# Performance work log

Measured on AMD Instinct MI355X. Metric: run time of the kernel, lower is better.

Reference implementation:

```python
import jax, jax.numpy as jnp
import numpy as np

B, H, S, DK, DV = 2, 16, 2048, 64, 64


def setup_inputs() -> dict:
    key = jax.random.key(0)
    kq, kk, kv = jax.random.split(key, 3)
    queries = jax.random.normal(kq, (B, H, S, DK), dtype=jnp.float32)
    keys = jax.random.normal(kk, (B, H, S, DK), dtype=jnp.float32)
    values = jax.random.normal(kv, (B, H, S, DV), dtype=jnp.float32)
    # causal boolean mask, broadcastable over batch and heads
    mask = jnp.tril(jnp.ones((S, S), dtype=bool))[None, None, :, :]
    return {"queries": queries, "keys": keys, "values": values, "d_k": DK, "mask": mask}


def reference(queries, keys, values, d_k, mask):
    scale = 1.0 / jnp.sqrt(jnp.float32(d_k))
    # scores: [B, H, S, S]
    scores = jnp.einsum("bhqd,bhkd->bhqk", queries, keys) * scale
    mask_f = mask.astype(jnp.float32)
    scores = scores + (-1e9) * (1.0 - mask_f)
    weights = jax.nn.softmax(scores, axis=-1)
    # second mask step from the original: min(|mask|, |weights|)
    weights = jnp.minimum(jnp.abs(mask_f), jnp.abs(weights))
    return jnp.einsum("bhqk,bhkd->bhqd", weights, values)
```

## Files before the change

kernel.cpp:

```cpp
#include <hip/hip_runtime.h>
#include <hip/hip_bf16.h>

#define B_ 2
#define H_ 16
#define S_ 2048
#define D_ 64

typedef __attribute__((ext_vector_type(8))) short bf16x8;
typedef __attribute__((ext_vector_type(8))) unsigned short u16x8;
typedef __attribute__((ext_vector_type(4))) unsigned int u32x4;
typedef __attribute__((ext_vector_type(4))) float f32x4;
typedef unsigned short ushort_t;

#define SCALE 0.18033688011112042f

__device__ __forceinline__ unsigned short f2bf(float x) {
  unsigned int u = __builtin_bit_cast(unsigned int, x);
  unsigned int r = (u + 0x7FFFu + ((u >> 16) & 1u)) >> 16;
  return (unsigned short)r;
}

__device__ __forceinline__ unsigned int cvt_pk_bf16(float lo, float hi) {
  unsigned int r;
  asm("v_cvt_pk_bf16_f32 %0, %1, %2" : "=v"(r) : "v"(lo), "v"(hi));
  return r;
}

__device__ __forceinline__ float fast_exp2(float x) {
  float r;
  asm("v_exp_f32 %0, %1" : "=v"(r) : "v"(x));
  return r;
}

__device__ __forceinline__ float fmax3(float a, float b, float c) {
  return fmaxf(fmaxf(a, b), c);
}

__device__ __forceinline__ int sigma_row(int rl) {
  return (rl & 0x23) | ((rl & 0x0C) << 1) | ((rl & 0x10) >> 2);
}

#define GLL16(gp, lp)                                                          \
  __builtin_amdgcn_global_load_lds(                                            \
      (const __attribute__((address_space(1))) unsigned int*)(gp),             \
      (__attribute__((address_space(3))) unsigned int*)(lp), 16, 0, 0)

__global__ void prepack(const float* __restrict__ Kf, const float* __restrict__ Vf,
                        ushort_t* __restrict__ Kg, ushort_t* __restrict__ Vtg) {
  const int blk = blockIdx.x;
  const int tid = threadIdx.x;
  const int bh = blk >> 5, t = blk & 31;
  const float* srcK = Kf + ((size_t)bh * S_ + (size_t)t * 64) * D_;
  const float* srcV = Vf + ((size_t)bh * S_ + (size_t)t * 64) * D_;
  ushort_t* dK = Kg + (size_t)blk * 4096;
  ushort_t* dV = Vtg + (size_t)blk * 4096;
  for (int is = 0; is < 2; ++is) {
    const int e = is * 2048 + tid * 8;
    {
      const int rl = e >> 6, pos = (e >> 3) & 7, ch = pos ^ (rl & 7);
      const float* sp = srcK + sigma_row(rl) * 64 + ch * 8;
      float4 a = *(const float4*)sp;
      float4 b = *(const float4*)(sp + 4);
      u16x8 w;
      w[0] = f2bf(a.x); w[1] = f2bf(a.y); w[2] = f2bf(a.z); w[3] = f2bf(a.w);
      w[4] = f2bf(b.x); w[5] = f2bf(b.y); w[6] = f2bf(b.z); w[7] = f2bf(b.w);
      *(u16x8*)(dK + e) = w;
    }
    {
      const int d0 = e >> 6, pos = (e >> 3) & 7, ch = pos ^ (d0 & 7);
      u16x8 w;
      for (int i = 0; i < 8; ++i) w[i] = f2bf(srcV[(size_t)(ch * 8 + i) * 64 + d0]);
      *(u16x8*)(dV + e) = w;
    }
  }
}

__launch_bounds__(256, 5)
__global__ void attn_split(const float* __restrict__ Qf, const ushort_t* __restrict__ Kg,
                           const ushort_t* __restrict__ Vtg, float* __restrict__ O,
                           float* __restrict__ PO, float* __restrict__ ML) {
  const int bh = blockIdx.x;
  const int y = blockIdx.y;
  int qt, c;
  if (y == 0) { qt = 15; c = 0; }
  else if (y <= 16) { qt = 15 + y; c = 0; }
  else if (y == 17) { qt = 31; c = 1; }
  else { const int p = y - 18, k = 15 - (p >> 1);
         if (p & 1) { qt = k + 15; c = 1; } else { qt = k - 1; c = 0; } }
  const int t0 = c << 4;
  const int t1 = (qt < t0 + 15) ? qt : (t0 + 15);

  const int tid = threadIdx.x;
  const int wave = tid >> 6, lane = tid & 63;
  const int col = lane & 15, g = lane >> 4;

  __shared__ __align__(16) ushort_t Kl[2][64][64];
  __shared__ __align__(16) ushort_t Vt[2][64][64];

  const int qrow = qt * 64 + wave * 16 + col;
  bf16x8 qf[2];
  {
    const float* Qh = Qf + (size_t)bh * S_ * D_;
    for (int kk = 0; kk < 2; ++kk) {
      const float* p = Qh + (size_t)qrow * 64 + kk * 32 + g * 8;
      float4 a = *(const float4*)p;
      float4 b = *(const float4*)(p + 4);
      float v[8] = {a.x, a.y, a.z, a.w, b.x, b.y, b.z, b.w};
      bf16x8 w;
      for (int i = 0; i < 8; ++i) w[i] = (short)f2bf(v[i] * SCALE);
      qf[kk] = w;
    }
  }

  f32x4 acc[4] = {};
  float m_ = -INFINITY, l_ = 0.0f;

  const int ch0 = (g ^ (col & 7)) << 3;
  const int ch1 = ((4 | g) ^ (col & 7)) << 3;

  auto STAGE = [&](int t, int b) {
    const ushort_t* kg = Kg + ((size_t)(bh * 32 + t)) * 4096;
    const ushort_t* vg = Vtg + ((size_t)(bh * 32 + t)) * 4096;
    GLL16(kg + tid * 8,        &Kl[b][0][0] + tid * 8);
    GLL16(kg + 2048 + tid * 8, &Kl[b][0][0] + 2048 + tid * 8);
    GLL16(vg + tid * 8,        &Vt[b][0][0] + tid * 8);
    GLL16(vg + 2048 + tid * 8, &Vt[b][0][0] + 2048 + tid * 8);
  };

  auto COMPUTE = [&](int b, bool diag) {
    f32x4 s[4] = {{0,0,0,0},{0,0,0,0},{0,0,0,0},{0,0,0,0}};
    __builtin_amdgcn_s_setprio(1);
    #pragma unroll
    for (int nt = 0; nt < 4; ++nt) {
      const ushort_t* row = &Kl[b][nt * 16 + col][0];
      const bf16x8 kf0 = *(const bf16x8*)(row + ch0);
      const bf16x8 kf1 = *(const bf16x8*)(row + ch1);
      s[nt] = __builtin_amdgcn_mfma_f32_16x16x32_bf16(kf0, qf[0], s[nt], 0, 0, 0);
      s[nt] = __builtin_amdgcn_mfma_f32_16x16x32_bf16(kf1, qf[1], s[nt], 0, 0, 0);
    }
    __builtin_amdgcn_s_setprio(0);
    if (diag) {
      const int qloc = wave * 16 + col;
      #pragma unroll
      for (int nt = 0; nt < 4; ++nt) {
        const int tau_base = 32 * (nt >> 1) + 4 * (nt & 1) + 8 * g;
        #pragma unroll
        for (int r = 0; r < 4; ++r)
          if (tau_base + r > qloc) s[nt][r] = -INFINITY;
      }
    }
    float a0 = fmax3(s[0][0], s[0][1], s[0][2]);
    float a1 = fmax3(s[0][3], s[1][0], s[1][1]);
    float a2 = fmax3(s[1][2], s[1][3], s[2][0]);
    float a3 = fmax3(s[2][1], s[2][2], s[2][3]);
    float a4 = fmax3(s[3][0], s[3][1], s[3][2]);
    float pm = fmax3(fmax3(a0, a1, s[3][3]), fmax3(a2, a3, a4), -INFINITY);
    pm = fmaxf(pm, __shfl_xor(pm, 16));
    pm = fmaxf(pm, __shfl_xor(pm, 32));
    float fac = 1.0f;
    if (!__all(pm - m_ <= 8.0f)) {
      const float mn = fmaxf(m_, pm);
      fac = fast_exp2(m_ - mn);
      m_ = mn;
      #pragma unroll
      for (int nt = 0; nt < 4; ++nt) acc[nt] *= fac;
    }
    #pragma unroll
    for (int nt = 0; nt < 4; ++nt)
      #pragma unroll
      for (int r = 0; r < 4; ++r) s[nt][r] = fast_exp2(s[nt][r] - m_);
    float b0 = (s[0][0] + s[0][1]) + (s[0][2] + s[0][3]);
    float b1 = (s[1][0] + s[1][1]) + (s[1][2] + s[1][3]);
    float b2 = (s[2][0] + s[2][1]) + (s[2][2] + s[2][3]);
    float b3 = (s[3][0] + s[3][1]) + (s[3][2] + s[3][3]);
    l_ = l_ * fac + ((b0 + b1) + (b2 + b3));
    u32x4 w0, w1;
    w0[0] = cvt_pk_bf16(s[0][0], s[0][1]); w0[1] = cvt_pk_bf16(s[0][2], s[0][3]);
    w0[2] = cvt_pk_bf16(s[1][0], s[1][1]); w0[3] = cvt_pk_bf16(s[1][2], s[1][3]);
    w1[0] = cvt_pk_bf16(s[2][0], s[2][1]); w1[1] = cvt_pk_bf16(s[2][2], s[2][3]);
    w1[2] = cvt_pk_bf16(s[3][0], s[3][1]); w1[3] = cvt_pk_bf16(s[3][2], s[3][3]);
    const bf16x8 pf0 = __builtin_bit_cast(bf16x8, w0);
    const bf16x8 pf1 = __builtin_bit_cast(bf16x8, w1);
    __builtin_amdgcn_s_setprio(1);
    #pragma unroll
    for (int nt = 0; nt < 4; ++nt) {
      const ushort_t* row = &Vt[b][nt * 16 + col][0];
      const bf16x8 vf0 = *(const bf16x8*)(row + ch0);
      const bf16x8 vf1 = *(const bf16x8*)(row + ch1);
      acc[nt] = __builtin_amdgcn_mfma_f32_16x16x32_bf16(vf0, pf0, acc[nt], 0, 0, 0);
      acc[nt] = __builtin_amdgcn_mfma_f32_16x16x32_bf16(vf1, pf1, acc[nt], 0, 0, 0);
    }
    __builtin_amdgcn_s_setprio(0);
  };

  int cur = 0;
  STAGE(t0, 0);
  __syncthreads();
  for (int t = t0; t <= t1; ++t) {
    if (t < t1) STAGE(t + 1, cur ^ 1);
    COMPUTE(cur, t == qt);
    __syncthreads();
    cur ^= 1;
  }

  float lsum = l_;
  lsum += __shfl_xor(lsum, 16);
  lsum += __shfl_xor(lsum, 32);
  const int rowloc = wave * 16 + col;
  if (qt <= 15) {
    const float inv = 1.0f / lsum;
    float* dst = O + (size_t)bh * S_ * D_ + (size_t)qrow * 64;
    #pragma unroll
    for (int nt = 0; nt < 4; ++nt) {
      f32x4 v = acc[nt];
      v *= inv;
      *(f32x4*)(dst + nt * 16 + 4 * g) = v;
    }
  } else {
    float* po = PO + (size_t)((((bh << 4) + (qt - 16)) << 1) + c) * 4096;
    #pragma unroll
    for (int nt = 0; nt < 4; ++nt)
      *(f32x4*)(po + rowloc * 64 + nt * 16 + 4 * g) = acc[nt];
    if (g == 0) {
      float* ml = ML + (size_t)((((bh << 4) + (qt - 16)) << 1) + c) * 128 + rowloc * 2;
      ml[0] = m_;
      ml[1] = lsum;
    }
  }
}

__global__ void merge_partials(const float* __restrict__ PO, const float* __restrict__ ML,
                               float* __restrict__ O) {
  const int bh = blockIdx.x;
  const int q16 = blockIdx.y;
  const int tid = threadIdx.x;
  const int r = tid >> 2, d0 = (tid & 3) << 4;
  const size_t base = (size_t)((bh << 4) + q16) << 1;
  const float* ml0 = ML + base * 128 + r * 2;
  const float* ml1 = ML + (base + 1) * 128 + r * 2;
  const float m0 = ml0[0], l0 = ml0[1], m1 = ml1[0], l1 = ml1[1];
  const float M = fmaxf(m0, m1);
  const float w0 = fast_exp2(m0 - M), w1 = fast_exp2(m1 - M);
  const float inv = 1.0f / (w0 * l0 + w1 * l1);
  const float a = w0 * inv, b = w1 * inv;
  const float* p0 = PO + base * 4096 + r * 64 + d0;
  const float* p1 = PO + (base + 1) * 4096 + r * 64 + d0;
  float* out = O + ((size_t)bh * S_ + (size_t)(16 + q16) * 64 + r) * 64 + d0;
  #pragma unroll
  for (int j = 0; j < 4; ++j) {
    float4 x = *(const float4*)(p0 + 4 * j);
    float4 y = *(const float4*)(p1 + 4 * j);
    float4 o;
    o.x = a * x.x + b * y.x; o.y = a * x.y + b * y.y;
    o.z = a * x.z + b * y.z; o.w = a * x.w + b * y.w;
    *(float4*)(out + 4 * j) = o;
  }
}

template <int PRE>
__launch_bounds__(256, 4)
__global__ void attn6(const float* __restrict__ Qf, const float* __restrict__ Kf,
                      const float* __restrict__ Vf, const ushort_t* __restrict__ Kg,
                      const ushort_t* __restrict__ Vtg, float* __restrict__ O) {
  const int bh = blockIdx.x;
  const int qt = 31 - blockIdx.y;
  const int tid = threadIdx.x;
  const int wave = tid >> 6, lane = tid & 63;
  const int col = lane & 15, g = lane >> 4;
  __shared__ __align__(16) ushort_t Kl[2][64][64];
  __shared__ __align__(16) ushort_t Vt[2][64][64];
  float* Oh = O + (size_t)bh * S_ * D_;
  const int qrow = qt * 64 + wave * 16 + col;
  bf16x8 qf[2];
  {
    const float* Qh = Qf + (size_t)bh * S_ * D_;
    for (int kk = 0; kk < 2; ++kk) {
      const float* p = Qh + (size_t)qrow * 64 + kk * 32 + g * 8;
      float4 a = *(const float4*)p;
      float4 b = *(const float4*)(p + 4);
      float v[8] = {a.x, a.y, a.z, a.w, b.x, b.y, b.z, b.w};
      bf16x8 w;
      for (int i = 0; i < 8; ++i) w[i] = (short)f2bf(v[i] * SCALE);
      qf[kk] = w;
    }
  }
  f32x4 acc[4] = {};
  float m_ = -INFINITY, l_ = 0.0f;
  const int ch0 = (g ^ (col & 7)) << 3;
  const int ch1 = ((4 | g) ^ (col & 7)) << 3;
  auto STAGE = [&](int t, int b) {
    if (PRE) {
      const ushort_t* kg = Kg + ((size_t)(bh * 32 + t)) * 4096;
      const ushort_t* vg = Vtg + ((size_t)(bh * 32 + t)) * 4096;
      GLL16(kg + tid * 8,        &Kl[b][0][0] + tid * 8);
      GLL16(kg + 2048 + tid * 8, &Kl[b][0][0] + 2048 + tid * 8);
      GLL16(vg + tid * 8,        &Vt[b][0][0] + tid * 8);
      GLL16(vg + 2048 + tid * 8, &Vt[b][0][0] + 2048 + tid * 8);
    } else {
      const float* Kh = Kf + (size_t)bh * S_ * D_;
      const float* Vh = Vf + (size_t)bh * S_ * D_;
      {
        const int rl = tid >> 2;
        const int c0 = (tid & 3) << 4;
        const float* src = Kh + ((size_t)(t * 64 + sigma_row(rl))) * 64 + c0;
        for (int jj = 0; jj < 2; ++jj) {
          float4 x = *(const float4*)(src + jj * 8);
          float4 y = *(const float4*)(src + jj * 8 + 4);
          u16x8 w;
          w[0] = f2bf(x.x); w[1] = f2bf(x.y); w[2] = f2bf(x.z); w[3] = f2bf(x.w);
          w[4] = f2bf(y.x); w[5] = f2bf(y.y); w[6] = f2bf(y.z); w[7] = f2bf(y.w);
          const int ch = (c0 >> 3) + jj;
          *(u16x8*)&Kl[b][rl][(ch ^ (rl & 7)) << 3] = w;
        }
      }
      {
        const int c = tid & 63;
        const int r0 = (tid >> 6) << 4;
        const float* src = Vh + ((size_t)(t * 64 + r0)) * 64 + c;
        for (int jj = 0; jj < 2; ++jj) {
          u16x8 w;
          for (int i = 0; i < 8; ++i) w[i] = f2bf(src[(size_t)(jj * 8 + i) * 64]);
          const int ch = (r0 >> 3) + jj;
          *(u16x8*)&Vt[b][c][(ch ^ (c & 7)) << 3] = w;
        }
      }
    }
  };
  auto COMPUTE = [&](int b, bool diag) {
    f32x4 s[4] = {{0,0,0,0},{0,0,0,0},{0,0,0,0},{0,0,0,0}};
    __builtin_amdgcn_s_setprio(1);
    for (int nt = 0; nt < 4; ++nt) {
      const ushort_t* row = &Kl[b][nt * 16 + col][0];
      const bf16x8 kf0 = *(const bf16x8*)(row + ch0);
      const bf16x8 kf1 = *(const bf16x8*)(row + ch1);
      s[nt] = __builtin_amdgcn_mfma_f32_16x16x32_bf16(kf0, qf[0], s[nt], 0, 0, 0);
      s[nt] = __builtin_amdgcn_mfma_f32_16x16x32_bf16(kf1, qf[1], s[nt], 0, 0, 0);
    }
    __builtin_amdgcn_s_setprio(0);
    if (diag) {
      const int qloc = wave * 16 + col;
      for (int nt = 0; nt < 4; ++nt) {
        const int tau_base = 32 * (nt >> 1) + 4 * (nt & 1) + 8 * g;
        for (int r = 0; r < 4; ++r)
          if (tau_base + r > qloc) s[nt][r] = -INFINITY;
      }
    }
    float pm = fmaxf(fmaxf(fmaxf(s[0][0], s[0][1]), fmaxf(s[0][2], s[0][3])),
                     fmaxf(fmaxf(s[1][0], s[1][1]), fmaxf(s[1][2], s[1][3])));
    pm = fmaxf(pm, fmaxf(fmaxf(fmaxf(s[2][0], s[2][1]), fmaxf(s[2][2], s[2][3])),
                         fmaxf(fmaxf(s[3][0], s[3][1]), fmaxf(s[3][2], s[3][3]))));
    pm = fmaxf(pm, __shfl_xor(pm, 16));
    pm = fmaxf(pm, __shfl_xor(pm, 32));
    float fac = 1.0f;
    if (!__all(pm - m_ <= 8.0f)) {
      const float mn = fmaxf(m_, pm);
      fac = fast_exp2(m_ - mn);
      m_ = mn;
      for (int nt = 0; nt < 4; ++nt) acc[nt] *= fac;
    }
    float sum = 0.0f;
    for (int nt = 0; nt < 4; ++nt)
      for (int r = 0; r < 4; ++r) {
        const float p = fast_exp2(s[nt][r] - m_);
        s[nt][r] = p;
        sum += p;
      }
    l_ = l_ * fac + sum;
    u32x4 t0, t1;
    t0[0] = cvt_pk_bf16(s[0][0], s[0][1]); t0[1] = cvt_pk_bf16(s[0][2], s[0][3]);
    t0[2] = cvt_pk_bf16(s[1][0], s[1][1]); t0[3] = cvt_pk_bf16(s[1][2], s[1][3]);
    t1[0] = cvt_pk_bf16(s[2][0], s[2][1]); t1[1] = cvt_pk_bf16(s[2][2], s[2][3]);
    t1[2] = cvt_pk_bf16(s[3][0], s[3][1]); t1[3] = cvt_pk_bf16(s[3][2], s[3][3]);
    const bf16x8 pf0 = __builtin_bit_cast(bf16x8, t0);
    const bf16x8 pf1 = __builtin_bit_cast(bf16x8, t1);
    __builtin_amdgcn_s_setprio(1);
    for (int nt = 0; nt < 4; ++nt) {
      const ushort_t* row = &Vt[b][nt * 16 + col][0];
      const bf16x8 vf0 = *(const bf16x8*)(row + ch0);
      const bf16x8 vf1 = *(const bf16x8*)(row + ch1);
      acc[nt] = __builtin_amdgcn_mfma_f32_16x16x32_bf16(vf0, pf0, acc[nt], 0, 0, 0);
      acc[nt] = __builtin_amdgcn_mfma_f32_16x16x32_bf16(vf1, pf1, acc[nt], 0, 0, 0);
    }
    __builtin_amdgcn_s_setprio(0);
  };
  int cur = 0;
  STAGE(0, 0);
  __syncthreads();
  for (int t = 0; t <= qt; ++t) {
    if (t < qt) STAGE(t + 1, cur ^ 1);
    COMPUTE(cur, t == qt);
    __syncthreads();
    cur ^= 1;
  }
  float lsum = l_;
  lsum += __shfl_xor(lsum, 16);
  lsum += __shfl_xor(lsum, 32);
  const float inv = 1.0f / lsum;
  float* dst = Oh + (size_t)qrow * 64;
  for (int nt = 0; nt < 4; ++nt) {
    f32x4 v = acc[nt];
    v *= inv;
    *(f32x4*)(dst + nt * 16 + 4 * g) = v;
  }
}

extern "C" void kernel_launch(void* const* d_in, const int* in_sizes, int n_in,
                              void* d_out, int out_size, void* d_ws, size_t ws_size,
                              hipStream_t stream) {
  const float* Q = (const float*)d_in[0];
  const float* K = (const float*)d_in[1];
  const float* V = (const float*)d_in[2];
  float* O = (float*)d_out;
  const size_t NE = (size_t)B_ * H_ * S_ * D_;
  const size_t needK = 2 * NE * sizeof(ushort_t);
  const size_t PO_elems = 32ull * 16 * 2 * 4096;
  const size_t ML_elems = 32ull * 16 * 2 * 128;
  const size_t needSplit = needK + (PO_elems + ML_elems) * sizeof(float);
  if (ws_size >= needSplit) {
    ushort_t* kg = (ushort_t*)d_ws;
    float* PO = (float*)((char*)d_ws + needK);
    float* ML = PO + PO_elems;
    prepack<<<1024, 256, 0, stream>>>(K, V, kg, kg + NE);
    attn_split<<<dim3(32, 48), 256, 0, stream>>>(Q, kg, kg + NE, O, PO, ML);
    merge_partials<<<dim3(32, 16), 256, 0, stream>>>(PO, ML, O);
  } else if (ws_size >= needK) {
    ushort_t* kg = (ushort_t*)d_ws;
    prepack<<<1024, 256, 0, stream>>>(K, V, kg, kg + NE);
    attn6<1><<<dim3(32, 32), 256, 0, stream>>>(Q, K, V, kg, kg + NE, O);
  } else {
    attn6<0><<<dim3(32, 32), 256, 0, stream>>>(Q, K, V, nullptr, nullptr, O);
  }
}
```

Before: 55.95 us.

## Shrink key tile to 32 rows to halve LDS and raise occupancy

Changes the split-K attention kernel to process 32-key tiles instead of 64. The prepack layout for K and transposed V is adjusted to match, and the causal mask and loop bounds move to 32-key granularity. LDS use per block is halved and launch bounds are raised to 8 blocks per CU, aiming for more latency hiding and finer diagonal masking. The cost is twice as many loop iterations, barriers and softmax rescale checks per block, with fewer MFMAs between syncs. The intermediate prepack fallback path is removed.

```diff
diff --git a/kernel.cpp b/kernel.cpp
--- a/kernel.cpp
+++ b/kernel.cpp
@@ -36,8 +36,8 @@
   return fmaxf(fmaxf(a, b), c);
 }
 
-__device__ __forceinline__ int sigma_row(int rl) {
-  return (rl & 0x23) | ((rl & 0x0C) << 1) | ((rl & 0x10) >> 2);
+__device__ __forceinline__ int sigma32(int lr) {
+  return (lr & 3) | ((lr & 0x0C) << 1) | ((lr & 0x10) >> 2);
 }
 
 #define GLL16(gp, lp)                                                          \
@@ -45,40 +45,38 @@
       (const __attribute__((address_space(1))) unsigned int*)(gp),             \
       (__attribute__((address_space(3))) unsigned int*)(lp), 16, 0, 0)
 
-__global__ void prepack(const float* __restrict__ Kf, const float* __restrict__ Vf,
-                        ushort_t* __restrict__ Kg, ushort_t* __restrict__ Vtg) {
+__global__ void prepack32(const float* __restrict__ Kf, const float* __restrict__ Vf,
+                          ushort_t* __restrict__ Kg, ushort_t* __restrict__ Vtg) {
   const int blk = blockIdx.x;
   const int tid = threadIdx.x;
-  const int bh = blk >> 5, t = blk & 31;
-  const float* srcK = Kf + ((size_t)bh * S_ + (size_t)t * 64) * D_;
-  const float* srcV = Vf + ((size_t)bh * S_ + (size_t)t * 64) * D_;
-  ushort_t* dK = Kg + (size_t)blk * 4096;
-  ushort_t* dV = Vtg + (size_t)blk * 4096;
-  for (int is = 0; is < 2; ++is) {
-    const int e = is * 2048 + tid * 8;
-    {
-      const int rl = e >> 6, pos = (e >> 3) & 7, ch = pos ^ (rl & 7);
-      const float* sp = srcK + sigma_row(rl) * 64 + ch * 8;
-      float4 a = *(const float4*)sp;
-      float4 b = *(const float4*)(sp + 4);
-      u16x8 w;
-      w[0] = f2bf(a.x); w[1] = f2bf(a.y); w[2] = f2bf(a.z); w[3] = f2bf(a.w);
-      w[4] = f2bf(b.x); w[5] = f2bf(b.y); w[6] = f2bf(b.z); w[7] = f2bf(b.w);
-      *(u16x8*)(dK + e) = w;
-    }
-    {
-      const int d0 = e >> 6, pos = (e >> 3) & 7, ch = pos ^ (d0 & 7);
-      u16x8 w;
-      for (int i = 0; i < 8; ++i) w[i] = f2bf(srcV[(size_t)(ch * 8 + i) * 64 + d0]);
-      *(u16x8*)(dV + e) = w;
-    }
-  }
-}
-
-__launch_bounds__(256, 5)
-__global__ void attn_split(const float* __restrict__ Qf, const ushort_t* __restrict__ Kg,
-                           const ushort_t* __restrict__ Vtg, float* __restrict__ O,
-                           float* __restrict__ PO, float* __restrict__ ML) {
+  const int bh = blk >> 6, kt = blk & 63;
+  const float* srcK = Kf + ((size_t)bh * S_ + (size_t)kt * 32) * D_;
+  const float* srcV = Vf + ((size_t)bh * S_ + (size_t)kt * 32) * D_;
+  ushort_t* dK = Kg + (size_t)blk * 2048;
+  ushort_t* dV = Vtg + (size_t)blk * 2048;
+  const int e = tid * 8;
+  {
+    const int lr = e >> 6, pos = (e >> 3) & 7, ch = pos ^ (lr & 7);
+    const float* sp = srcK + sigma32(lr) * 64 + ch * 8;
+    float4 a = *(const float4*)sp;
+    float4 b = *(const float4*)(sp + 4);
+    u16x8 w;
+    w[0] = f2bf(a.x); w[1] = f2bf(a.y); w[2] = f2bf(a.z); w[3] = f2bf(a.w);
+    w[4] = f2bf(b.x); w[5] = f2bf(b.y); w[6] = f2bf(b.z); w[7] = f2bf(b.w);
+    *(u16x8*)(dK + e) = w;
+  }
+  {
+    const int d0 = e >> 5, pos2 = (e >> 3) & 3, ch2 = pos2 ^ (d0 & 3);
+    u16x8 w;
+    for (int i = 0; i < 8; ++i) w[i] = f2bf(srcV[(size_t)(ch2 * 8 + i) * 64 + d0]);
+    *(u16x8*)(dV + e) = w;
+  }
+}
+
+__launch_bounds__(256, 8)
+__global__ void attn_s32(const float* __restrict__ Qf, const ushort_t* __restrict__ Kg,
+                         const ushort_t* __restrict__ Vtg, float* __restrict__ O,
+                         float* __restrict__ PO, float* __restrict__ ML) {
   const int bh = blockIdx.x;
   const int y = blockIdx.y;
   int qt, c;
@@ -87,15 +85,16 @@
   else if (y == 17) { qt = 31; c = 1; }
   else { const int p = y - 18, k = 15 - (p >> 1);
          if (p & 1) { qt = k + 15; c = 1; } else { qt = k - 1; c = 0; } }
-  const int t0 = c << 4;
-  const int t1 = (qt < t0 + 15) ? qt : (t0 + 15);
+  const int t0k = c << 5;
+  const int tEnd = 2 * qt + 1;
+  const int t1k = (tEnd < t0k + 31) ? tEnd : (t0k + 31);
 
   const int tid = threadIdx.x;
   const int wave = tid >> 6, lane = tid & 63;
   const int col = lane & 15, g = lane >> 4;
 
-  __shared__ __align__(16) ushort_t Kl[2][64][64];
-  __shared__ __align__(16) ushort_t Vt[2][64][64];
+  __shared__ __align__(16) ushort_t Kl[2][32][64];
+  __shared__ __align__(16) ushort_t Vt[2][64][32];
 
   const int qrow = qt * 64 + wave * 16 + col;
   bf16x8 qf[2];
@@ -117,21 +116,20 @@
 
   const int ch0 = (g ^ (col & 7)) << 3;
   const int ch1 = ((4 | g) ^ (col & 7)) << 3;
-
-  auto STAGE = [&](int t, int b) {
-    const ushort_t* kg = Kg + ((size_t)(bh * 32 + t)) * 4096;
-    const ushort_t* vg = Vtg + ((size_t)(bh * 32 + t)) * 4096;
-    GLL16(kg + tid * 8,        &Kl[b][0][0] + tid * 8);
-    GLL16(kg + 2048 + tid * 8, &Kl[b][0][0] + 2048 + tid * 8);
-    GLL16(vg + tid * 8,        &Vt[b][0][0] + tid * 8);
-    GLL16(vg + 2048 + tid * 8, &Vt[b][0][0] + 2048 + tid * 8);
+  const int chV = (g ^ (col & 3)) << 3;
+
+  auto STAGE = [&](int kt, int b) {
+    const ushort_t* kg = Kg + ((size_t)(bh * 64 + kt)) * 2048;
+    const ushort_t* vg = Vtg + ((size_t)(bh * 64 + kt)) * 2048;
+    GLL16(kg + tid * 8, &Kl[b][0][0] + tid * 8);
+    GLL16(vg + tid * 8, &Vt[b][0][0] + tid * 8);
   };
 
-  auto COMPUTE = [&](int b, bool diag) {
-    f32x4 s[4] = {{0,0,0,0},{0,0,0,0},{0,0,0,0},{0,0,0,0}};
+  auto COMPUTE = [&](int kt, int b, bool diag) {
+    f32x4 s[2] = {{0,0,0,0},{0,0,0,0}};
     __builtin_amdgcn_s_setprio(1);
     #pragma unroll
-    for (int nt = 0; nt < 4; ++nt) {
+    for (int nt = 0; nt < 2; ++nt) {
       const ushort_t* row = &Kl[b][nt * 16 + col][0];
       const bf16x8 kf0 = *(const bf16x8*)(row + ch0);
       const bf16x8 kf1 = *(const bf16x8*)(row + ch1);
@@ -140,21 +138,16 @@
     }
     __builtin_amdgcn_s_setprio(0);
     if (diag) {
-      const int qloc = wave * 16 + col;
+      const int qg = qt * 64 + wave * 16 + col - 32 * kt - 8 * g;
       #pragma unroll
-      for (int nt = 0; nt < 4; ++nt) {
-        const int tau_base = 32 * (nt >> 1) + 4 * (nt & 1) + 8 * g;
+      for (int nt = 0; nt < 2; ++nt)
         #pragma unroll
         for (int r = 0; r < 4; ++r)
-          if (tau_base + r > qloc) s[nt][r] = -INFINITY;
-      }
-    }
-    float a0 = fmax3(s[0][0], s[0][1], s[0][2]);
-    float a1 = fmax3(s[0][3], s[1][0], s[1][1]);
-    float a2 = fmax3(s[1][2], s[1][3], s[2][0]);
-    float a3 = fmax3(s[2][1], s[2][2], s[2][3]);
-    float a4 = fmax3(s[3][0], s[3][1], s[3][2]);
-    float pm = fmax3(fmax3(a0, a1, s[3][3]), fmax3(a2, a3, a4), -INFINITY);
+          if (4 * nt + r > qg) s[nt][r] = -INFINITY;
+    }
+    float pm = fmax3(fmax3(s[0][0], s[0][1], s[0][2]),
+                     fmax3(s[0][3], s[1][0], s[1][1]),
+                     fmaxf(fmaxf(s[1][2], s[1][3]), -INFINITY));
     pm = fmaxf(pm, __shfl_xor(pm, 16));
     pm = fmaxf(pm, __shfl_xor(pm, 32));
     float fac = 1.0f;
@@ -166,39 +159,32 @@
       for (int nt = 0; nt < 4; ++nt) acc[nt] *= fac;
     }
     #pragma unroll
-    for (int nt = 0; nt < 4; ++nt)
+    for (int nt = 0; nt < 2; ++nt)
       #pragma unroll
       for (int r = 0; r < 4; ++r) s[nt][r] = fast_exp2(s[nt][r] - m_);
-    float b0 = (s[0][0] + s[0][1]) + (s[0][2] + s[0][3]);
-    float b1 = (s[1][0] + s[1][1]) + (s[1][2] + s[1][3]);
-    float b2 = (s[2][0] + s[2][1]) + (s[2][2] + s[2][3]);
-    float b3 = (s[3][0] + s[3][1]) + (s[3][2] + s[3][3]);
-    l_ = l_ * fac + ((b0 + b1) + (b2 + b3));
-    u32x4 w0, w1;
-    w0[0] = cvt_pk_bf16(s[0][0], s[0][1]); w0[1] = cvt_pk_bf16(s[0][2], s[0][3]);
-    w0[2] = cvt_pk_bf16(s[1][0], s[1][1]); w0[3] = cvt_pk_bf16(s[1][2], s[1][3]);
-    w1[0] = cvt_pk_bf16(s[2][0], s[2][1]); w1[1] = cvt_pk_bf16(s[2][2], s[2][3]);
-    w1[2] = cvt_pk_bf16(s[3][0], s[3][1]); w1[3] = cvt_pk_bf16(s[3][2], s[3][3]);
-    const bf16x8 pf0 = __builtin_bit_cast(bf16x8, w0);
-    const bf16x8 pf1 = __builtin_bit_cast(bf16x8, w1);
+    const float b0 = (s[0][0] + s[0][1]) + (s[0][2] + s[0][3]);
+    const float b1 = (s[1][0] + s[1][1]) + (s[1][2] + s[1][3]);
+    l_ = l_ * fac + (b0 + b1);
+    u32x4 w;
+    w[0] = cvt_pk_bf16(s[0][0], s[0][1]); w[1] = cvt_pk_bf16(s[0][2], s[0][3]);
+    w[2] = cvt_pk_bf16(s[1][0], s[1][1]); w[3] = cvt_pk_bf16(s[1][2], s[1][3]);
+    const bf16x8 pf = __builtin_bit_cast(bf16x8, w);
     __builtin_amdgcn_s_setprio(1);
     #pragma unroll
     for (int nt = 0; nt < 4; ++nt) {
-      const ushort_t* row = &Vt[b][nt * 16 + col][0];
-      const bf16x8 vf0 = *(const bf16x8*)(row + ch0);
-      const bf16x8 vf1 = *(const bf16x8*)(row + ch1);
-      acc[nt] = __builtin_amdgcn_mfma_f32_16x16x32_bf16(vf0, pf0, acc[nt], 0, 0, 0);
-      acc[nt] = __builtin_amdgcn_mfma_f32_16x16x32_bf16(vf1, pf1, acc[nt], 0, 0, 0);
+      const bf16x8 vf = *(const bf16x8*)(&Vt[b][nt * 16 + col][0] + chV);
+      acc[nt] = __builtin_amdgcn_mfma_f32_16x16x32_bf16(vf, pf, acc[nt], 0, 0, 0);
     }
     __builtin_amdgcn_s_setprio(0);
   };
 
   int cur = 0;
-  STAGE(t0, 0);
+  STAGE(t0k, 0);
   __syncthreads();
-  for (int t = t0; t <= t1; ++t) {
-    if (t < t1) STAGE(t + 1, cur ^ 1);
-    COMPUTE(cur, t == qt);
+  const int diag0 = 2 * qt;
+  for (int kt = t0k; kt <= t1k; ++kt) {
+    if (kt < t1k) STAGE(kt + 1, cur ^ 1);
+    COMPUTE(kt, cur, kt >= diag0);
     __syncthreads();
     cur ^= 1;
   }
@@ -257,11 +243,12 @@
   }
 }
 
-template <int PRE>
+__device__ __forceinline__ int sigma_row64(int rl) {
+  return (rl & 0x23) | ((rl & 0x0C) << 1) | ((rl & 0x10) >> 2);
+}
 __launch_bounds__(256, 4)
-__global__ void attn6(const float* __restrict__ Qf, const float* __restrict__ Kf,
-                      const float* __restrict__ Vf, const ushort_t* __restrict__ Kg,
-                      const ushort_t* __restrict__ Vtg, float* __restrict__ O) {
+__global__ void attn_fb(const float* __restrict__ Qf, const float* __restrict__ Kf,
+                        const float* __restrict__ Vf, float* __restrict__ O) {
   const int bh = blockIdx.x;
   const int qt = 31 - blockIdx.y;
   const int tid = threadIdx.x;
@@ -269,7 +256,6 @@
   const int col = lane & 15, g = lane >> 4;
   __shared__ __align__(16) ushort_t Kl[2][64][64];
   __shared__ __align__(16) ushort_t Vt[2][64][64];
-  float* Oh = O + (size_t)bh * S_ * D_;
   const int qrow = qt * 64 + wave * 16 + col;
   bf16x8 qf[2];
   {
@@ -289,46 +275,36 @@
   const int ch0 = (g ^ (col & 7)) << 3;
   const int ch1 = ((4 | g) ^ (col & 7)) << 3;
   auto STAGE = [&](int t, int b) {
-    if (PRE) {
-      const ushort_t* kg = Kg + ((size_t)(bh * 32 + t)) * 4096;
-      const ushort_t* vg = Vtg + ((size_t)(bh * 32 + t)) * 4096;
-      GLL16(kg + tid * 8,        &Kl[b][0][0] + tid * 8);
-      GLL16(kg + 2048 + tid * 8, &Kl[b][0][0] + 2048 + tid * 8);
-      GLL16(vg + tid * 8,        &Vt[b][0][0] + tid * 8);
-      GLL16(vg + 2048 + tid * 8, &Vt[b][0][0] + 2048 + tid * 8);
-    } else {
-      const float* Kh = Kf + (size_t)bh * S_ * D_;
-      const float* Vh = Vf + (size_t)bh * S_ * D_;
-      {
-        const int rl = tid >> 2;
-        const int c0 = (tid & 3) << 4;
-        const float* src = Kh + ((size_t)(t * 64 + sigma_row(rl))) * 64 + c0;
-        for (int jj = 0; jj < 2; ++jj) {
-          float4 x = *(const float4*)(src + jj * 8);
-          float4 y = *(const float4*)(src + jj * 8 + 4);
-          u16x8 w;
-          w[0] = f2bf(x.x); w[1] = f2bf(x.y); w[2] = f2bf(x.z); w[3] = f2bf(x.w);
-          w[4] = f2bf(y.x); w[5] = f2bf(y.y); w[6] = f2bf(y.z); w[7] = f2bf(y.w);
-          const int ch = (c0 >> 3) + jj;
-          *(u16x8*)&Kl[b][rl][(ch ^ (rl & 7)) << 3] = w;
-        }
+    const float* Kh = Kf + (size_t)bh * S_ * D_;
+    const float* Vh = Vf + (size_t)bh * S_ * D_;
+    {
+      const int rl = tid >> 2;
+      const int c0 = (tid & 3) << 4;
+      const float* src = Kh + ((size_t)(t * 64 + sigma_row64(rl))) * 64 + c0;
+      for (int jj = 0; jj < 2; ++jj) {
+        float4 x = *(const float4*)(src + jj * 8);
+        float4 y = *(const float4*)(src + jj * 8 + 4);
+        u16x8 w;
+        w[0] = f2bf(x.x); w[1] = f2bf(x.y); w[2] = f2bf(x.z); w[3] = f2bf(x.w);
+        w[4] = f2bf(y.x); w[5] = f2bf(y.y); w[6] = f2bf(y.z); w[7] = f2bf(y.w);
+        const int ch = (c0 >> 3) + jj;
+        *(u16x8*)&Kl[b][rl][(ch ^ (rl & 7)) << 3] = w;
       }
-      {
-        const int c = tid & 63;
-        const int r0 = (tid >> 6) << 4;
-        const float* src = Vh + ((size_t)(t * 64 + r0)) * 64 + c;
-        for (int jj = 0; jj < 2; ++jj) {
-          u16x8 w;
-          for (int i = 0; i < 8; ++i) w[i] = f2bf(src[(size_t)(jj * 8 + i) * 64]);
-          const int ch = (r0 >> 3) + jj;
-          *(u16x8*)&Vt[b][c][(ch ^ (c & 7)) << 3] = w;
-        }
+    }
+    {
+      const int cc = tid & 63;
+      const int r0 = (tid >> 6) << 4;
+      const float* src = Vh + ((size_t)(t * 64 + r0)) * 64 + cc;
+      for (int jj = 0; jj < 2; ++jj) {
+        u16x8 w;
+        for (int i = 0; i < 8; ++i) w[i] = f2bf(src[(size_t)(jj * 8 + i) * 64]);
+        const int ch = (r0 >> 3) + jj;
+        *(u16x8*)&Vt[b][cc][(ch ^ (cc & 7)) << 3] = w;
       }
     }
   };
   auto COMPUTE = [&](int b, bool diag) {
     f32x4 s[4] = {{0,0,0,0},{0,0,0,0},{0,0,0,0},{0,0,0,0}};
-    __builtin_amdgcn_s_setprio(1);
     for (int nt = 0; nt < 4; ++nt) {
       const ushort_t* row = &Kl[b][nt * 16 + col][0];
       const bf16x8 kf0 = *(const bf16x8*)(row + ch0);
@@ -336,19 +312,17 @@
       s[nt] = __builtin_amdgcn_mfma_f32_16x16x32_bf16(kf0, qf[0], s[nt], 0, 0, 0);
       s[nt] = __builtin_amdgcn_mfma_f32_16x16x32_bf16(kf1, qf[1], s[nt], 0, 0, 0);
     }
-    __builtin_amdgcn_s_setprio(0);
     if (diag) {
       const int qloc = wave * 16 + col;
       for (int nt = 0; nt < 4; ++nt) {
-        const int tau_base = 32 * (nt >> 1) + 4 * (nt & 1) + 8 * g;
+        const int tb = 32 * (nt >> 1) + 4 * (nt & 1) + 8 * g;
         for (int r = 0; r < 4; ++r)
-          if (tau_base + r > qloc) s[nt][r] = -INFINITY;
+          if (tb + r > qloc) s[nt][r] = -INFINITY;
       }
     }
-    float pm = fmaxf(fmaxf(fmaxf(s[0][0], s[0][1]), fmaxf(s[0][2], s[0][3])),
-                     fmaxf(fmaxf(s[1][0], s[1][1]), fmaxf(s[1][2], s[1][3])));
-    pm = fmaxf(pm, fmaxf(fmaxf(fmaxf(s[2][0], s[2][1]), fmaxf(s[2][2], s[2][3])),
-                         fmaxf(fmaxf(s[3][0], s[3][1]), fmaxf(s[3][2], s[3][3]))));
+    float pm = -INFINITY;
+    for (int nt = 0; nt < 4; ++nt)
+      for (int r = 0; r < 4; ++r) pm = fmaxf(pm, s[nt][r]);
     pm = fmaxf(pm, __shfl_xor(pm, 16));
     pm = fmaxf(pm, __shfl_xor(pm, 32));
     float fac = 1.0f;
@@ -373,7 +347,6 @@
     t1[2] = cvt_pk_bf16(s[3][0], s[3][1]); t1[3] = cvt_pk_bf16(s[3][2], s[3][3]);
     const bf16x8 pf0 = __builtin_bit_cast(bf16x8, t0);
     const bf16x8 pf1 = __builtin_bit_cast(bf16x8, t1);
-    __builtin_amdgcn_s_setprio(1);
     for (int nt = 0; nt < 4; ++nt) {
       const ushort_t* row = &Vt[b][nt * 16 + col][0];
       const bf16x8 vf0 = *(const bf16x8*)(row + ch0);
@@ -381,7 +354,6 @@
       acc[nt] = __builtin_amdgcn_mfma_f32_16x16x32_bf16(vf0, pf0, acc[nt], 0, 0, 0);
       acc[nt] = __builtin_amdgcn_mfma_f32_16x16x32_bf16(vf1, pf1, acc[nt], 0, 0, 0);
     }
-    __builtin_amdgcn_s_setprio(0);
   };
   int cur = 0;
   STAGE(0, 0);
@@ -396,7 +368,7 @@
   lsum += __shfl_xor(lsum, 16);
   lsum += __shfl_xor(lsum, 32);
   const float inv = 1.0f / lsum;
-  float* dst = Oh + (size_t)qrow * 64;
+  float* dst = O + (size_t)bh * S_ * D_ + (size_t)qrow * 64;
   for (int nt = 0; nt < 4; ++nt) {
     f32x4 v = acc[nt];
     v *= inv;
@@ -420,14 +392,10 @@
     ushort_t* kg = (ushort_t*)d_ws;
     float* PO = (float*)((char*)d_ws + needK);
     float* ML = PO + PO_elems;
-    prepack<<<1024, 256, 0, stream>>>(K, V, kg, kg + NE);
-    attn_split<<<dim3(32, 48), 256, 0, stream>>>(Q, kg, kg + NE, O, PO, ML);
+    prepack32<<<2048, 256, 0, stream>>>(K, V, kg, kg + NE);
+    attn_s32<<<dim3(32, 48), 256, 0, stream>>>(Q, kg, kg + NE, O, PO, ML);
     merge_partials<<<dim3(32, 16), 256, 0, stream>>>(PO, ML, O);
-  } else if (ws_size >= needK) {
-    ushort_t* kg = (ushort_t*)d_ws;
-    prepack<<<1024, 256, 0, stream>>>(K, V, kg, kg + NE);
-    attn6<1><<<dim3(32, 32), 256, 0, stream>>>(Q, K, V, kg, kg + NE, O);
   } else {
-    attn6<0><<<dim3(32, 32), 256, 0, stream>>>(Q, K, V, nullptr, nullptr, O);
-  }
-}
+    attn_fb<<<dim3(32, 32), 256, 0, stream>>>(Q, K, V, O);
+  }
+}
```

New measurement: 54.83 us. 2.0% less time.
